# Kernel optimization log

Measured on AMD Instinct MI355X. Metric: run time of the kernel, lower is better.

The kernel has to match this reference:

```python
import jax, jax.numpy as jnp
import numpy as np

N_QUBITS = 6

def _apply_1q(state, U, w):
    # state: [B] + [2]*6 complex; U: [2,2] complex
    ax = 1 + w
    s = jnp.moveaxis(state, ax, -1)
    s = jnp.einsum('...j,ij->...i', s, U)
    return jnp.moveaxis(s, -1, ax)

def _apply_cnot(state, ctrl, tgt):
    ca, ta = 1 + ctrl, 1 + tgt
    s = jnp.moveaxis(state, (ca, ta), (1, 2))  # [B,2,2,...]
    s = jnp.stack([s[:, 0], s[:, 1, ::-1]], axis=1)
    return jnp.moveaxis(s, (1, 2), (ca, ta))

def _rot(phi, theta, omega):
    # PennyLane Rot = RZ(omega) RY(theta) RZ(phi)
    c, s = jnp.cos(theta / 2), jnp.sin(theta / 2)
    return jnp.stack([
        jnp.stack([jnp.exp(-0.5j * (phi + omega)) * c, -jnp.exp(0.5j * (phi - omega)) * s]),
        jnp.stack([jnp.exp(-0.5j * (phi - omega)) * s, jnp.exp(0.5j * (phi + omega)) * c]),
    ])

def _quantum(xq, qw):
    B = xq.shape[0]
    # AngleEmbedding RY: product state, per-qubit amplitudes [cos(x/2), sin(x/2)]
    amps = jnp.stack([jnp.cos(xq / 2), jnp.sin(xq / 2)], axis=-1)  # [B,6,2]
    state = amps[:, 0]
    for i in range(1, N_QUBITS):
        state = jnp.einsum('b...,bj->b...j', state, amps[:, i])
    state = state.astype(jnp.complex64)  # [B,2,2,2,2,2,2]
    # StronglyEntanglingLayers: per layer Rot on each wire, then CNOT ring of range r
    n_layers = qw.shape[0]
    for l in range(n_layers):
        for w in range(N_QUBITS):
            U = _rot(qw[l, w, 0], qw[l, w, 1], qw[l, w, 2])
            state = _apply_1q(state, U, w)
        r = (l % (N_QUBITS - 1)) + 1  # default ranges
        for w in range(N_QUBITS):
            state = _apply_cnot(state, w, (w + r) % N_QUBITS)
    probs = jnp.abs(state) ** 2
    zs = []
    for w in range(N_QUBITS):
        axes = tuple(a for a in range(1, N_QUBITS + 1) if a != 1 + w)
        p = jnp.sum(probs, axis=axes)  # [B,2]
        zs.append(p[:, 0] - p[:, 1])
    return jnp.stack(zs, axis=-1)  # [B,6]

def setup_inputs() -> dict:
    key = jax.random.key(0)
    ks = jax.random.split(key, 10)
    B = 16384
    return {
        'xc': jax.random.normal(ks[0], (B, 2048), jnp.float32),
        'xq': jax.random.uniform(ks[1], (B, N_QUBITS), jnp.float32),
        'W1': jax.random.normal(ks[2], (64, 2048), jnp.float32) * 0.02,
        'b1': jnp.zeros((64,), jnp.float32),
        'qw': jax.random.uniform(ks[3], (3, N_QUBITS, 3), jnp.float32, 0.0, 2 * np.pi),
        'Wq': jax.random.normal(ks[4], (16, N_QUBITS), jnp.float32) * 0.3,
        'bq': jnp.zeros((16,), jnp.float32),
        'Wf': jax.random.normal(ks[5], (3, 80), jnp.float32) * 0.1,
        'bf': jnp.zeros((3,), jnp.float32),
    }

def reference(xc, xq, W1, b1, qw, Wq, bq, Wf, bf):
    c = jax.nn.relu(xc @ W1.T + b1)                 # [B,64]
    q = _quantum(xq, qw) @ Wq.T + bq                # [B,16]
    return jnp.concatenate([c, q], axis=1) @ Wf.T + bf  # [B,3]
```

## Files before the change

### kernel.cpp

```cpp
#include <hip/hip_runtime.h>
#include <hip/hip_bf16.h>

#define NQ 6

typedef __attribute__((ext_vector_type(8))) short short8;
typedef __attribute__((ext_vector_type(4))) float floatx4;

#define WS_MQ_F   8192
#define WS_CQ_F   (8192+18)
#define WS_W1BF_B 36864

typedef const __attribute__((address_space(1))) void gvoid_t;
typedef __attribute__((address_space(3))) void lvoid_t;

__global__ __launch_bounds__(64) void prep_kernel(
    const float* __restrict__ qw, int n_layers,
    const float* __restrict__ W1, const float* __restrict__ Wq,
    const float* __restrict__ bq, const float* __restrict__ Wf,
    const float* __restrict__ bf, float* __restrict__ ws_f,
    short* __restrict__ w1bf)
{
    const int blk  = blockIdx.x;
    const int lane = threadIdx.x;

    if (blk == 0) {
        if (lane < 18) {
            int j = lane / 6, wi = lane % 6;
            float s = 0.f;
            for (int m = 0; m < 16; ++m) s += Wf[j*80 + 64 + m] * Wq[m*6 + wi];
            ws_f[WS_MQ_F + lane] = s;
        } else if (lane < 21) {
            int j = lane - 18;
            float s = bf[j];
            for (int m = 0; m < 16; ++m) s += Wf[j*80 + 64 + m] * bq[m];
            ws_f[WS_CQ_F + j] = s;
        }
    } else if (blk <= 64) {
        const int j = blk - 1;
        float re = (lane == j) ? 1.f : 0.f;
        float im = 0.f;
        for (int l = 0; l < n_layers; ++l) {
            for (int w = 0; w < NQ; ++w) {
                const float* g = qw + (l*NQ + w)*3;
                float phi = g[0], th = g[1], om = g[2];
                float c, s;  __sincosf(0.5f*th, &s, &c);
                float sa, ca; __sincosf(0.5f*(phi+om), &sa, &ca);
                float sb, cb; __sincosf(0.5f*(phi-om), &sb, &cb);
                float u00r =  c*ca, u00i = -c*sa;
                float u01r = -s*cb, u01i = -s*sb;
                float u10r =  s*cb, u10i = -s*sb;
                float u11r =  c*ca, u11i =  c*sa;
                int p = 5 - w, mask = 1 << p;
                float pre = __shfl_xor(re, mask, 64);
                float pim = __shfl_xor(im, mask, 64);
                int b = (lane >> p) & 1;
                float mr = b ? u11r : u00r, mi = b ? u11i : u00i;
                float pr = b ? u10r : u01r, pi = b ? u10i : u01i;
                float nre = mr*re - mi*im + pr*pre - pi*pim;
                float nim = mr*im + mi*re + pr*pim + pi*pre;
                re = nre; im = nim;
            }
            int r = l % (NQ-1) + 1;
            for (int w = 0; w < NQ; ++w) {
                int tgt = (w + r) % NQ;
                int tmask = 1 << (5 - tgt);
                float pre = __shfl_xor(re, tmask, 64);
                float pim = __shfl_xor(im, tmask, 64);
                int cs = (lane >> (5 - w)) & 1;
                re = cs ? pre : re;
                im = cs ? pim : im;
            }
        }
        ws_f[(lane*64 + j)*2 + 0] = re;
        ws_f[(lane*64 + j)*2 + 1] = im;
    } else {
        int idx = (blk - 65)*512 + lane*8;
        if (idx < 64*2048) {
            float4 a0 = *(const float4*)(W1 + idx);
            float4 a1 = *(const float4*)(W1 + idx + 4);
            union { short8 v; __hip_bfloat162 h[4]; } u;
            float2 f;
            f.x=a0.x; f.y=a0.y; u.h[0] = __float22bfloat162_rn(f);
            f.x=a0.z; f.y=a0.w; u.h[1] = __float22bfloat162_rn(f);
            f.x=a1.x; f.y=a1.y; u.h[2] = __float22bfloat162_rn(f);
            f.x=a1.z; f.y=a1.w; u.h[3] = __float22bfloat162_rn(f);
            *(short8*)(w1bf + idx) = u.v;
        }
    }
}

__device__ __forceinline__ short8 cvt_bf16x8(float4 a0, float4 a1) {
    union { short8 v; __hip_bfloat162 h[4]; } u;
    float2 f;
    f.x=a0.x; f.y=a0.y; u.h[0] = __float22bfloat162_rn(f);
    f.x=a0.z; f.y=a0.w; u.h[1] = __float22bfloat162_rn(f);
    f.x=a1.x; f.y=a1.y; u.h[2] = __float22bfloat162_rn(f);
    f.x=a1.z; f.y=a1.w; u.h[3] = __float22bfloat162_rn(f);
    return u.v;
}

__global__ __launch_bounds__(512, 4) void fused_kernel(
    const float* __restrict__ xq, const float2* __restrict__ U,
    const float* __restrict__ ws_f,
    const float* __restrict__ xc, const short* __restrict__ w1bf,
    const float* __restrict__ b1, const float* __restrict__ Wf,
    float* __restrict__ out)
{
    const int tid  = threadIdx.x;
    const int lane = tid & 63;
    const int t    = __builtin_amdgcn_readfirstlane((int)(tid >> 6));
    const int blk  = blockIdx.x;

    __shared__ __align__(16) char Aring[3*8192];
    __shared__ __align__(16) char Bring[3*8192];
    __shared__ float zbuf[8][32][6];
    __shared__ float cl[32][65];
    __shared__ float qres[32][3];

    const int wr = t >> 2, wc = t & 3;
    const int rA = t*4 + (lane >> 4);
    const int gA = lane & 15;
    const int uA = gA >> 1;
    const float* asrcA = xc + (size_t)(blk*32 + rA)*2048
                       + ((uA ^ (rA & 7)) << 3) + ((gA & 1) << 2);
    const int colB = t*8 + (lane >> 3);
    const int gB = lane & 7;
    const short* bsrcB = w1bf + colB*2048 + ((gB ^ (colB & 7)) << 3);
    const int a_l  = lane >> 4;
    const int arow = wr*16 + (lane & 15);
    const int bcol = wc*16 + (lane & 15);
    const int aoff0 = arow*256 + (((0*4 + a_l) ^ (arow & 7)) << 5);
    const int aoff1 = arow*256 + (((1*4 + a_l) ^ (arow & 7)) << 5);
    const int boff0 = bcol*128 + (((0*4 + a_l) ^ (bcol & 7)) << 4);
    const int boff1 = bcol*128 + (((1*4 + a_l) ^ (bcol & 7)) << 4);

    const float* xrow = xq + (size_t)(blk*32 + (lane & 31))*6;
    float2 xq01 = *(const float2*)(xrow);
    float2 xq23 = *(const float2*)(xrow + 2);
    float2 xq45 = *(const float2*)(xrow + 4);

    __builtin_amdgcn_global_load_lds((gvoid_t*)(asrcA + 0*64),
        (lvoid_t*)(Aring + 0*8192 + t*1024), 16, 0, 0);
    __builtin_amdgcn_global_load_lds((gvoid_t*)(bsrcB + 0*64),
        (lvoid_t*)(Bring + 0*8192 + t*1024), 16, 0, 0);
    __builtin_amdgcn_global_load_lds((gvoid_t*)(asrcA + 1*64),
        (lvoid_t*)(Aring + 1*8192 + t*1024), 16, 0, 0);
    __builtin_amdgcn_global_load_lds((gvoid_t*)(bsrcB + 1*64),
        (lvoid_t*)(Bring + 1*8192 + t*1024), 16, 0, 0);

    {
        const float xs[6] = {xq01.x, xq01.y, xq23.x, xq23.y, xq45.x, xq45.y};
        float ah[8], al[8];
        ah[0] = 1.f;
        #pragma unroll
        for (int q = 0; q < 3; ++q) {
            float c, s; __sincosf(0.5f*xs[q], &s, &c);
            const int sz = 1 << q;
            #pragma unroll
            for (int m = sz-1; m >= 0; --m) {
                float v = ah[m];
                ah[2*m+1] = v*s;
                ah[2*m+0] = v*c;
            }
        }
        al[0] = 1.f;
        #pragma unroll
        for (int q = 0; q < 3; ++q) {
            float c, s; __sincosf(0.5f*xs[3+q], &s, &c);
            const int sz = 1 << q;
            #pragma unroll
            for (int m = sz-1; m >= 0; --m) {
                float v = al[m];
                al[2*m+1] = v*s;
                al[2*m+0] = v*c;
            }
        }

        float zp[6] = {0,0,0,0,0,0};
        const float2* Urow = U + t*8*64;
        for (int ii = 0; ii < 8; ++ii) {
            float rr = 0.f, ri = 0.f;
            #pragma unroll
            for (int jh = 0; jh < 8; ++jh) {
                float sr = 0.f, si = 0.f;
                #pragma unroll
                for (int jl = 0; jl < 8; ++jl) {
                    float2 u = Urow[ii*64 + jh*8 + jl];
                    sr += u.x * al[jl];
                    si += u.y * al[jl];
                }
                rr += ah[jh] * sr;
                ri += ah[jh] * si;
            }
            float p = rr*rr + ri*ri;
            int i = t*8 + ii;
            #pragma unroll
            for (int w = 0; w < 6; ++w) zp[w] += ((i >> (5-w)) & 1) ? -p : p;
        }
        if (lane < 32) {
            #pragma unroll
            for (int w = 0; w < 6; ++w) zbuf[t][lane][w] = zp[w];
        }
    }
    __syncthreads();
    if (t == 0 && lane < 32) {
        float z[6];
        #pragma unroll
        for (int w = 0; w < 6; ++w) {
            float s = 0.f;
            #pragma unroll
            for (int sbi = 0; sbi < 8; ++sbi) s += zbuf[sbi][lane][w];
            z[w] = s;
        }
        #pragma unroll
        for (int j = 0; j < 3; ++j) {
            float v = ws_f[WS_CQ_F + j];
            #pragma unroll
            for (int w = 0; w < 6; ++w) v += ws_f[WS_MQ_F + j*6 + w] * z[w];
            qres[lane][j] = v;
        }
    }
    __syncthreads();

    floatx4 acc = {0,0,0,0};

    #pragma unroll
    for (int c = 0; c < 32; ++c) {
        const int rs = c % 3;

        if (c + 2 < 32) {
            const int wslot = (c + 2) % 3;
            __builtin_amdgcn_global_load_lds((gvoid_t*)(asrcA + (c+2)*64),
                (lvoid_t*)(Aring + wslot*8192 + t*1024), 16, 0, 0);
            __builtin_amdgcn_global_load_lds((gvoid_t*)(bsrcB + (c+2)*64),
                (lvoid_t*)(Bring + wslot*8192 + t*1024), 16, 0, 0);
        }

        const char* ab = Aring + rs*8192;
        const char* bb = Bring + rs*8192;
        float4 f00 = *(const float4*)(ab + aoff0);
        float4 f01 = *(const float4*)(ab + aoff0 + 16);
        float4 f10 = *(const float4*)(ab + aoff1);
        float4 f11 = *(const float4*)(ab + aoff1 + 16);
        short8 bv0 = *(const short8*)(bb + boff0);
        short8 bv1 = *(const short8*)(bb + boff1);
        acc = __builtin_amdgcn_mfma_f32_16x16x32_bf16(cvt_bf16x8(f00, f01), bv0, acc, 0, 0, 0);
        acc = __builtin_amdgcn_mfma_f32_16x16x32_bf16(cvt_bf16x8(f10, f11), bv1, acc, 0, 0, 0);

        if (c < 31) {
            __builtin_amdgcn_sched_barrier(0);
            asm volatile("s_waitcnt lgkmcnt(0)" ::: "memory");
            if (c <= 29) {
                asm volatile("s_waitcnt vmcnt(2)" ::: "memory");
            } else {
                asm volatile("s_waitcnt vmcnt(0)" ::: "memory");
            }
            __builtin_amdgcn_s_barrier();
            __builtin_amdgcn_sched_barrier(0);
        }
    }
    __syncthreads();

    const int rbase = wr*16 + a_l*4;
    const float bb1 = b1[bcol];
    #pragma unroll
    for (int r = 0; r < 4; ++r)
        cl[rbase + r][bcol] = fmaxf(acc[r] + bb1, 0.f);
    __syncthreads();

    const int rr2 = lane & 31;
    if (t < 3 && lane < 32) {
        float v = 0.f;
        #pragma unroll
        for (int col = 0; col < 64; ++col) v += Wf[t*80 + col] * cl[rr2][col];
        int g = blk*32 + rr2;
        out[(size_t)g*3 + t] = v + qres[rr2][t];
    }
}

extern "C" void kernel_launch(void* const* d_in, const int* in_sizes, int n_in,
                              void* d_out, int out_size, void* d_ws, size_t ws_size,
                              hipStream_t stream) {
    const float* xc = (const float*)d_in[0];
    const float* xq = (const float*)d_in[1];
    const float* W1 = (const float*)d_in[2];
    const float* b1 = (const float*)d_in[3];
    const float* qw = (const float*)d_in[4];
    const float* Wq = (const float*)d_in[5];
    const float* bq = (const float*)d_in[6];
    const float* Wf = (const float*)d_in[7];
    const float* bf = (const float*)d_in[8];
    float* out = (float*)d_out;

    const int B = in_sizes[1] / NQ;
    const int n_layers = in_sizes[4] / (NQ * 3);

    char* ws = (char*)d_ws;
    float*  ws_f  = (float*)ws;
    float2* U     = (float2*)ws;
    short*  w1bf  = (short*)(ws + WS_W1BF_B);

    prep_kernel<<<dim3(321), dim3(64), 0, stream>>>(qw, n_layers, W1, Wq, bq, Wf, bf, ws_f, w1bf);
    fused_kernel<<<dim3(B/32), dim3(512), 0, stream>>>(xq, U, ws_f, xc, w1bf, b1, Wf, out);
}
```

Before: 237.6 us.

## Load A operand directly to registers and give each wave a private B ring

The xc (A) tiles are now loaded straight from global memory into registers with double buffering, and the shared-LDS A ring is dropped. Each wave fetches its own copy of its W1 bf16 slice into a private 3-slot LDS ring, so the per-iteration workgroup barrier and lgkmcnt wait are removed. The aim is to cut LDS traffic and barrier stalls in the K loop. The cost is duplicated B fetches across waves that share a column group, more registers in flight, and waits that depend on vmcnt accounting.

```diff
diff --git a/kernel.cpp b/kernel.cpp
--- a/kernel.cpp
+++ b/kernel.cpp
@@ -111,42 +111,27 @@
     const int t    = __builtin_amdgcn_readfirstlane((int)(tid >> 6));
     const int blk  = blockIdx.x;
 
-    __shared__ __align__(16) char Aring[3*8192];
-    __shared__ __align__(16) char Bring[3*8192];
+    __shared__ __align__(16) char Bbuf[8*3*2048];
     __shared__ float zbuf[8][32][6];
     __shared__ float cl[32][65];
     __shared__ float qres[32][3];
 
     const int wr = t >> 2, wc = t & 3;
-    const int rA = t*4 + (lane >> 4);
-    const int gA = lane & 15;
-    const int uA = gA >> 1;
-    const float* asrcA = xc + (size_t)(blk*32 + rA)*2048
-                       + ((uA ^ (rA & 7)) << 3) + ((gA & 1) << 2);
-    const int colB = t*8 + (lane >> 3);
-    const int gB = lane & 7;
-    const short* bsrcB = w1bf + colB*2048 + ((gB ^ (colB & 7)) << 3);
-    const int a_l  = lane >> 4;
-    const int arow = wr*16 + (lane & 15);
-    const int bcol = wc*16 + (lane & 15);
-    const int aoff0 = arow*256 + (((0*4 + a_l) ^ (arow & 7)) << 5);
-    const int aoff1 = arow*256 + (((1*4 + a_l) ^ (arow & 7)) << 5);
-    const int boff0 = bcol*128 + (((0*4 + a_l) ^ (bcol & 7)) << 4);
-    const int boff1 = bcol*128 + (((1*4 + a_l) ^ (bcol & 7)) << 4);
+    const int m16 = lane & 15;
+    const int kg  = lane >> 4;
+    const float* ap = xc + (size_t)(blk*32 + wr*16 + m16)*2048 + kg*8;
+    const int dq0 = 0*8 + (lane >> 3);
+    const int dq1 = 1*8 + (lane >> 3);
+    const short* bsrc0 = w1bf + (wc*16 + dq0)*2048 + (((lane & 7) ^ (dq0 & 7)) << 3);
+    const short* bsrc1 = w1bf + (wc*16 + dq1)*2048 + (((lane & 7) ^ (dq1 & 7)) << 3);
+    char* const bdst = Bbuf + t*6144;
+    const int boffs0 = t*6144 + m16*128 + (((0*4 + kg) ^ (m16 & 7)) << 4);
+    const int boffs1 = t*6144 + m16*128 + (((1*4 + kg) ^ (m16 & 7)) << 4);
 
     const float* xrow = xq + (size_t)(blk*32 + (lane & 31))*6;
     float2 xq01 = *(const float2*)(xrow);
     float2 xq23 = *(const float2*)(xrow + 2);
     float2 xq45 = *(const float2*)(xrow + 4);
-
-    __builtin_amdgcn_global_load_lds((gvoid_t*)(asrcA + 0*64),
-        (lvoid_t*)(Aring + 0*8192 + t*1024), 16, 0, 0);
-    __builtin_amdgcn_global_load_lds((gvoid_t*)(bsrcB + 0*64),
-        (lvoid_t*)(Bring + 0*8192 + t*1024), 16, 0, 0);
-    __builtin_amdgcn_global_load_lds((gvoid_t*)(asrcA + 1*64),
-        (lvoid_t*)(Aring + 1*8192 + t*1024), 16, 0, 0);
-    __builtin_amdgcn_global_load_lds((gvoid_t*)(bsrcB + 1*64),
-        (lvoid_t*)(Bring + 1*8192 + t*1024), 16, 0, 0);
 
     {
         const float xs[6] = {xq01.x, xq01.y, xq23.x, xq23.y, xq45.x, xq45.y};
@@ -220,52 +205,59 @@
             qres[lane][j] = v;
         }
     }
-    __syncthreads();
+
+    float4 pA[2][4];
+    #pragma unroll
+    for (int s = 0; s < 2; ++s) {
+        pA[s][0] = *(const float4*)(ap + s*64 + 0);
+        pA[s][1] = *(const float4*)(ap + s*64 + 4);
+        pA[s][2] = *(const float4*)(ap + s*64 + 32);
+        pA[s][3] = *(const float4*)(ap + s*64 + 36);
+        __builtin_amdgcn_global_load_lds((gvoid_t*)(bsrc0 + s*64),
+            (lvoid_t*)(bdst + (s%3)*2048 + 0*1024), 16, 0, 0);
+        __builtin_amdgcn_global_load_lds((gvoid_t*)(bsrc1 + s*64),
+            (lvoid_t*)(bdst + (s%3)*2048 + 1*1024), 16, 0, 0);
+    }
 
     floatx4 acc = {0,0,0,0};
 
     #pragma unroll
     for (int c = 0; c < 32; ++c) {
-        const int rs = c % 3;
+        if (c < 31) {
+            asm volatile("s_waitcnt vmcnt(6)" ::: "memory");
+        } else {
+            asm volatile("s_waitcnt vmcnt(0)" ::: "memory");
+        }
+        __builtin_amdgcn_sched_barrier(0);
+
+        short8 av0 = cvt_bf16x8(pA[c & 1][0], pA[c & 1][1]);
+        short8 av1 = cvt_bf16x8(pA[c & 1][2], pA[c & 1][3]);
 
         if (c + 2 < 32) {
-            const int wslot = (c + 2) % 3;
-            __builtin_amdgcn_global_load_lds((gvoid_t*)(asrcA + (c+2)*64),
-                (lvoid_t*)(Aring + wslot*8192 + t*1024), 16, 0, 0);
-            __builtin_amdgcn_global_load_lds((gvoid_t*)(bsrcB + (c+2)*64),
-                (lvoid_t*)(Bring + wslot*8192 + t*1024), 16, 0, 0);
-        }
-
-        const char* ab = Aring + rs*8192;
-        const char* bb = Bring + rs*8192;
-        float4 f00 = *(const float4*)(ab + aoff0);
-        float4 f01 = *(const float4*)(ab + aoff0 + 16);
-        float4 f10 = *(const float4*)(ab + aoff1);
-        float4 f11 = *(const float4*)(ab + aoff1 + 16);
-        short8 bv0 = *(const short8*)(bb + boff0);
-        short8 bv1 = *(const short8*)(bb + boff1);
-        acc = __builtin_amdgcn_mfma_f32_16x16x32_bf16(cvt_bf16x8(f00, f01), bv0, acc, 0, 0, 0);
-        acc = __builtin_amdgcn_mfma_f32_16x16x32_bf16(cvt_bf16x8(f10, f11), bv1, acc, 0, 0, 0);
-
-        if (c < 31) {
-            __builtin_amdgcn_sched_barrier(0);
-            asm volatile("s_waitcnt lgkmcnt(0)" ::: "memory");
-            if (c <= 29) {
-                asm volatile("s_waitcnt vmcnt(2)" ::: "memory");
-            } else {
-                asm volatile("s_waitcnt vmcnt(0)" ::: "memory");
-            }
-            __builtin_amdgcn_s_barrier();
-            __builtin_amdgcn_sched_barrier(0);
-        }
+            pA[c & 1][0] = *(const float4*)(ap + (c+2)*64 + 0);
+            pA[c & 1][1] = *(const float4*)(ap + (c+2)*64 + 4);
+            pA[c & 1][2] = *(const float4*)(ap + (c+2)*64 + 32);
+            pA[c & 1][3] = *(const float4*)(ap + (c+2)*64 + 36);
+            __builtin_amdgcn_global_load_lds((gvoid_t*)(bsrc0 + (c+2)*64),
+                (lvoid_t*)(bdst + ((c+2)%3)*2048 + 0*1024), 16, 0, 0);
+            __builtin_amdgcn_global_load_lds((gvoid_t*)(bsrc1 + (c+2)*64),
+                (lvoid_t*)(bdst + ((c+2)%3)*2048 + 1*1024), 16, 0, 0);
+        }
+
+        const char* bb = Bbuf;
+        short8 bv0 = *(const short8*)(bb + (c%3)*2048 + boffs0);
+        short8 bv1 = *(const short8*)(bb + (c%3)*2048 + boffs1);
+        acc = __builtin_amdgcn_mfma_f32_16x16x32_bf16(av0, bv0, acc, 0, 0, 0);
+        acc = __builtin_amdgcn_mfma_f32_16x16x32_bf16(av1, bv1, acc, 0, 0, 0);
     }
     __syncthreads();
 
-    const int rbase = wr*16 + a_l*4;
-    const float bb1 = b1[bcol];
+    const int rbase = wr*16 + kg*4;
+    const int ccol  = wc*16 + m16;
+    const float bb1 = b1[ccol];
     #pragma unroll
     for (int r = 0; r < 4; ++r)
-        cl[rbase + r][bcol] = fmaxf(acc[r] + bb1, 0.f);
+        cl[rbase + r][ccol] = fmaxf(acc[r] + bb1, 0.f);
     __syncthreads();
 
     const int rr2 = lane & 31;
```

Measured after the change: 251.3 us. +5.8%, slower.
